# Kernel tuning notes

Measured on AMD Instinct MI355X. Metric: run time of the kernel, lower is better.

Reference implementation:

```python
import jax, jax.numpy as jnp
import numpy as np

ALPHA, GAMMA = 0.25, 2.0
SPARSITY_PENALTY = 1.0
FOCAL_W, SPARSITY_W, CONC_W = 1.0, 0.8, 1.5
CONC_INNER_W = 1.0  # ConcentrationLoss(concentration_weight=1.0)


def setup_inputs() -> dict:
    key = jax.random.key(0)
    k1, k2 = jax.random.split(key)
    B, C, H, W = 16, 20, 256, 256
    pred = jax.random.normal(k1, (B, C, H, W), dtype=jnp.float32)
    target = (jax.random.uniform(k2, (B, C, H, W)) < 0.05).astype(jnp.float32)
    return {"pred": pred, "target": target}


def reference(pred, target):
    B, C, H, W = pred.shape
    p = jax.nn.sigmoid(pred)

    # ---- Focal loss ----
    is_pos = target == 1.0
    pt = jnp.where(is_pos, p, 1.0 - p)
    alpha_t = jnp.where(is_pos, ALPHA, 1.0 - ALPHA)
    focal = jnp.mean(-alpha_t * (1.0 - pt) ** GAMMA * jnp.log(pt + 1e-8))

    # ---- Sparsity loss ----
    sparsity = jnp.mean((pred - target) ** 2) + SPARSITY_PENALTY * jnp.mean(jnp.abs(pred))

    # ---- Concentration loss (vectorized over (b, c)) ----
    y = jnp.arange(H, dtype=jnp.float32)[:, None]   # [H,1]
    x = jnp.arange(W, dtype=jnp.float32)[None, :]   # [1,W]
    mass = target.sum(axis=(2, 3))                  # [B,C]
    valid = mass > 0
    safe_mass = jnp.where(valid, mass, 1.0)
    cy = jnp.einsum('bchw,hw->bc', target, jnp.broadcast_to(y, (H, W))) / safe_mass
    cx = jnp.einsum('bchw,hw->bc', target, jnp.broadcast_to(x, (H, W))) / safe_mass
    # squared distance to per-(b,c) target centroid: [B,C,H,W]
    dsq = (y[None, None] - cy[:, :, None, None]) ** 2 + (x[None, None] - cx[:, :, None, None]) ** 2
    per_sample = jnp.mean(p * dsq, axis=(2, 3))     # [B,C]
    n_valid = valid.sum()
    conc_sum = jnp.sum(jnp.where(valid, per_sample, 0.0))
    concentration = jnp.where(
        n_valid > 0,
        conc_sum / jnp.maximum(n_valid, 1).astype(jnp.float32),
        0.0,
    ) * CONC_INNER_W

    total = FOCAL_W * focal + SPARSITY_W * sparsity + CONC_W * concentration
    return total, focal, sparsity, concentration
```

## Files before the change

### kernel.cpp

```cpp
#include <hip/hip_runtime.h>
#include <math.h>

constexpr int Bn = 16, Cn = 20, Hn = 256, Wn = 256;
constexpr int BCn = Bn * Cn;
constexpr int HWn = Hn * Wn;
constexpr int SPLIT = 4;
constexpr int NBLK = BCn * SPLIT;
constexpr int CHUNK = HWn / SPLIT;
constexpr int TPB = 1024;
constexpr int NWAVE = TPB / 64;
constexpr int V4 = CHUNK / (TPB * 4);
constexpr int NSLOT = 10;

__device__ inline float wave_reduce(float v) {
    #pragma unroll
    for (int o = 32; o > 0; o >>= 1) v += __shfl_down(v, o, 64);
    return v;
}

__global__ __launch_bounds__(TPB, 4) void partials_kernel(
        const float* __restrict__ pred, const float* __restrict__ target,
        float* __restrict__ ws) {
    const int blk = blockIdx.x;
    const int bc = blk >> 2;
    const int chunk = blk & (SPLIT - 1);
    const long long base = (long long)bc * HWn + (long long)chunk * CHUNK;
    const float4* __restrict__ p4 = (const float4*)(pred + base);
    const float4* __restrict__ t4 = (const float4*)(target + base);
    const int tid = threadIdx.x;

    float acc[NSLOT];
    #pragma unroll
    for (int k = 0; k < NSLOT; k++) acc[k] = 0.f;

    const int e_base = chunk * CHUNK + tid * 4;
    const float x0 = (float)(e_base & 255);
    const float x1 = x0 + 1.f, x2 = x0 + 2.f, x3 = x0 + 3.f;
    const float xs[4]  = {x0, x1, x2, x3};
    const float xxs[4] = {x0 * x0, x1 * x1, x2 * x2, x3 * x3};
    float y = (float)(e_base >> 8);

    float4 pc = p4[tid];
    float4 tc = t4[tid];

    #pragma unroll
    for (int i = 0; i < V4; i++) {
        float4 pn, tn;
        if (i + 1 < V4) {
            pn = p4[(i + 1) * TPB + tid];
            tn = t4[(i + 1) * TPB + tid];
        }
        const float yy = y * y;
        const float pvals[4] = {pc.x, pc.y, pc.z, pc.w};
        const float tvals[4] = {tc.x, tc.y, tc.z, tc.w};
        #pragma unroll
        for (int j = 0; j < 4; j++) {
            const float v = pvals[j];
            const float t = tvals[j];
            const float x = xs[j];
            const float e = __expf(-v);
            const float p = __builtin_amdgcn_rcpf(1.0f + e);
            const bool pos = (t > 0.5f);
            const float lp = __logf(p);
            const float lpt = pos ? lp : lp - v;
            const float om = pos ? 1.0f - p : p;
            const float at = pos ? 0.25f : 0.75f;
            acc[7] = fmaf(at * lpt, om * om, acc[7]);
            const float d = v - t;
            acc[8] = fmaf(d, d, acc[8]);
            acc[9] += fabsf(v);
            acc[0] += t;
            acc[1] = fmaf(t, y, acc[1]);
            acc[2] = fmaf(t, x, acc[2]);
            acc[3] += p;
            acc[4] = fmaf(p, y, acc[4]);
            acc[5] = fmaf(p, x, acc[5]);
            acc[6] = fmaf(p, yy + xxs[j], acc[6]);
        }
        y += 16.0f;
        if (i + 1 < V4) { pc = pn; tc = tn; }
    }

    __shared__ float lds[NWAVE][NSLOT];
    const int lane = tid & 63, wave = tid >> 6;
    #pragma unroll
    for (int k = 0; k < NSLOT; k++) {
        const float r = wave_reduce(acc[k]);
        if (lane == 0) lds[wave][k] = r;
    }
    __syncthreads();
    if (tid < NSLOT) {
        float s = 0.f;
        #pragma unroll
        for (int w = 0; w < NWAVE; w++) s += lds[w][tid];
        ws[blk * NSLOT + tid] = s;
    }
}

__global__ __launch_bounds__(512) void finalize_kernel(
        const float* __restrict__ ws, float* __restrict__ out) {
    const int tid = threadIdx.x;

    float conc_sum = 0.f, nvalid = 0.f;
    if (tid < BCn) {
        float mass = 0, sty = 0, stx = 0, sp = 0, spy = 0, spx = 0, sprr = 0;
        for (int s = 0; s < SPLIT; s++) {
            const float* w = ws + (size_t)(tid * SPLIT + s) * NSLOT;
            mass += w[0]; sty += w[1]; stx += w[2]; sp += w[3];
            spy  += w[4]; spx += w[5]; sprr += w[6];
        }
        const bool valid = mass > 0.f;
        const float sm = valid ? mass : 1.0f;
        const float cy = sty / sm, cx = stx / sm;
        const float pdsq = sprr - 2.f * cy * spy - 2.f * cx * spx
                         + (cy * cy + cx * cx) * sp;
        conc_sum = valid ? (pdsq / (float)HWn) : 0.f;
        nvalid   = valid ? 1.f : 0.f;
    }

    float foc = 0.f, sq = 0.f, ab = 0.f;
    for (int blk = tid; blk < NBLK; blk += 512) {
        const float* w = ws + (size_t)blk * NSLOT;
        foc += w[7]; sq += w[8]; ab += w[9];
    }

    __shared__ float lds[8][5];
    const int lane = tid & 63, wave = tid >> 6;
    float vals[5] = {conc_sum, nvalid, foc, sq, ab};
    #pragma unroll
    for (int k = 0; k < 5; k++) {
        const float r = wave_reduce(vals[k]);
        if (lane == 0) lds[wave][k] = r;
    }
    __syncthreads();

    if (tid == 0) {
        float tot[5];
        #pragma unroll
        for (int k = 0; k < 5; k++) {
            float s = 0.f;
            #pragma unroll
            for (int w = 0; w < 8; w++) s += lds[w][k];
            tot[k] = s;
        }
        const float NTOT = (float)Bn * Cn * Hn * Wn;
        const float focal = -tot[2] / NTOT;
        const float sparsity = tot[3] / NTOT + tot[4] / NTOT;
        const float concentration =
            (tot[1] > 0.f) ? (tot[0] / fmaxf(tot[1], 1.f)) : 0.f;
        const float total = 1.0f * focal + 0.8f * sparsity + 1.5f * concentration;
        out[0] = total;
        out[1] = focal;
        out[2] = sparsity;
        out[3] = concentration;
    }
}

extern "C" void kernel_launch(void* const* d_in, const int* in_sizes, int n_in,
                              void* d_out, int out_size, void* d_ws, size_t ws_size,
                              hipStream_t stream) {
    const float* pred   = (const float*)d_in[0];
    const float* target = (const float*)d_in[1];
    float* out = (float*)d_out;
    float* ws  = (float*)d_ws;

    partials_kernel<<<NBLK, TPB, 0, stream>>>(pred, target, ws);
    finalize_kernel<<<1, 512, 0, stream>>>(ws, out);
}
```

Before: 189.3 us.

## Factor x/y moments out of inner loop, double-buffer loads, use 512-thread blocks

Each thread always sees the same four x columns, so per-column sums of t and p are accumulated and the x-weighted moments are formed once after the loop. The y-weighted moments use per-float4 row sums. The focal term is folded into a single squared scaled factor. Loads are prefetched two iterations ahead and the block shrinks to 512 threads with more iterations per thread. This cuts per-element ALU work in a memory-bound kernel and deepens load overlap, at the cost of slightly different float summation order and more registers.

```diff
diff --git a/kernel.cpp b/kernel.cpp
--- a/kernel.cpp
+++ b/kernel.cpp
@@ -7,7 +7,7 @@
 constexpr int SPLIT = 4;
 constexpr int NBLK = BCn * SPLIT;
 constexpr int CHUNK = HWn / SPLIT;
-constexpr int TPB = 1024;
+constexpr int TPB = 512;
 constexpr int NWAVE = TPB / 64;
 constexpr int V4 = CHUNK / (TPB * 4);
 constexpr int NSLOT = 10;
@@ -18,7 +18,7 @@
     return v;
 }
 
-__global__ __launch_bounds__(TPB, 4) void partials_kernel(
+__global__ __launch_bounds__(TPB) void partials_kernel(
         const float* __restrict__ pred, const float* __restrict__ target,
         float* __restrict__ ws) {
     const int blk = blockIdx.x;
@@ -29,57 +29,73 @@
     const float4* __restrict__ t4 = (const float4*)(target + base);
     const int tid = threadIdx.x;
 
-    float acc[NSLOT];
-    #pragma unroll
-    for (int k = 0; k < NSLOT; k++) acc[k] = 0.f;
+    float st[4] = {0.f, 0.f, 0.f, 0.f};
+    float sp[4] = {0.f, 0.f, 0.f, 0.f};
+    float sty = 0.f, spy = 0.f, spyy = 0.f;
+    float foc = 0.f, sq = 0.f, ab = 0.f;
 
     const int e_base = chunk * CHUNK + tid * 4;
     const float x0 = (float)(e_base & 255);
-    const float x1 = x0 + 1.f, x2 = x0 + 2.f, x3 = x0 + 3.f;
-    const float xs[4]  = {x0, x1, x2, x3};
-    const float xxs[4] = {x0 * x0, x1 * x1, x2 * x2, x3 * x3};
     float y = (float)(e_base >> 8);
 
-    float4 pc = p4[tid];
-    float4 tc = t4[tid];
+    float4 pa = p4[tid];
+    float4 ta = t4[tid];
+    float4 pb = p4[TPB + tid];
+    float4 tb = t4[TPB + tid];
 
     #pragma unroll
     for (int i = 0; i < V4; i++) {
         float4 pn, tn;
-        if (i + 1 < V4) {
-            pn = p4[(i + 1) * TPB + tid];
-            tn = t4[(i + 1) * TPB + tid];
+        if (i + 2 < V4) {
+            pn = p4[(i + 2) * TPB + tid];
+            tn = t4[(i + 2) * TPB + tid];
         }
         const float yy = y * y;
-        const float pvals[4] = {pc.x, pc.y, pc.z, pc.w};
-        const float tvals[4] = {tc.x, tc.y, tc.z, tc.w};
+        const float pvals[4] = {pa.x, pa.y, pa.z, pa.w};
+        const float tvals[4] = {ta.x, ta.y, ta.z, ta.w};
+        float pj[4];
         #pragma unroll
         for (int j = 0; j < 4; j++) {
             const float v = pvals[j];
             const float t = tvals[j];
-            const float x = xs[j];
             const float e = __expf(-v);
             const float p = __builtin_amdgcn_rcpf(1.0f + e);
+            pj[j] = p;
             const bool pos = (t > 0.5f);
             const float lp = __logf(p);
             const float lpt = pos ? lp : lp - v;
-            const float om = pos ? 1.0f - p : p;
-            const float at = pos ? 0.25f : 0.75f;
-            acc[7] = fmaf(at * lpt, om * om, acc[7]);
+            const float q = pos ? fmaf(-0.5f, p, 0.5f) : 0.8660254f * p;
+            foc = fmaf(q * q, lpt, foc);
             const float d = v - t;
-            acc[8] = fmaf(d, d, acc[8]);
-            acc[9] += fabsf(v);
-            acc[0] += t;
-            acc[1] = fmaf(t, y, acc[1]);
-            acc[2] = fmaf(t, x, acc[2]);
-            acc[3] += p;
-            acc[4] = fmaf(p, y, acc[4]);
-            acc[5] = fmaf(p, x, acc[5]);
-            acc[6] = fmaf(p, yy + xxs[j], acc[6]);
+            sq = fmaf(d, d, sq);
+            ab += fabsf(v);
+            st[j] += t;
+            sp[j] += p;
         }
-        y += 16.0f;
-        if (i + 1 < V4) { pc = pn; tc = tn; }
+        const float s_t = (tvals[0] + tvals[1]) + (tvals[2] + tvals[3]);
+        const float s_p = (pj[0] + pj[1]) + (pj[2] + pj[3]);
+        sty  = fmaf(s_t, y,  sty);
+        spy  = fmaf(s_p, y,  spy);
+        spyy = fmaf(s_p, yy, spyy);
+        y += 8.0f;
+        pa = pb; ta = tb;
+        if (i + 2 < V4) { pb = pn; tb = tn; }
     }
+
+    const float x1 = x0 + 1.f, x2 = x0 + 2.f, x3 = x0 + 3.f;
+    const float mass = (st[0] + st[1]) + (st[2] + st[3]);
+    const float Sp   = (sp[0] + sp[1]) + (sp[2] + sp[3]);
+    float stx  = x0 * st[0];
+    stx = fmaf(x1, st[1], stx); stx = fmaf(x2, st[2], stx); stx = fmaf(x3, st[3], stx);
+    float spx  = x0 * sp[0];
+    spx = fmaf(x1, sp[1], spx); spx = fmaf(x2, sp[2], spx); spx = fmaf(x3, sp[3], spx);
+    float spxx = (x0 * x0) * sp[0];
+    spxx = fmaf(x1 * x1, sp[1], spxx);
+    spxx = fmaf(x2 * x2, sp[2], spxx);
+    spxx = fmaf(x3 * x3, sp[3], spxx);
+    const float sprr = spyy + spxx;
+
+    float acc[NSLOT] = {mass, sty, stx, Sp, spy, spx, sprr, foc, sq, ab};
 
     __shared__ float lds[NWAVE][NSLOT];
     const int lane = tid & 63, wave = tid >> 6;
```

Result: no change. 191.8 us (+1.3%).
